# Kernel optimization log

Measured on AMD Instinct MI355X. Metric: run time of the kernel, lower is better.

## Reference

```python
import jax, jax.numpy as jnp
import numpy as np

NUM_HEADS = 4
NUM_GROUPS = 8
EPS = 1e-5


def setup_inputs() -> dict:
    key = jax.random.key(0)
    ks = jax.random.split(key, 7)
    c = 256
    return {
        "x": jax.random.normal(ks[0], (4, c, 64, 64), jnp.float32),
        "gn_w": jax.random.normal(ks[1], (c,), jnp.float32),
        "gn_b": jax.random.normal(ks[2], (c,), jnp.float32),
        "qkv_w": jax.random.normal(ks[3], (3 * c, c), jnp.float32) * (c ** -0.5),
        "qkv_b": jax.random.normal(ks[4], (3 * c,), jnp.float32) * 0.02,
        "proj_w": jax.random.normal(ks[5], (c, c), jnp.float32) * (c ** -0.5),
        "proj_b": jax.random.normal(ks[6], (c,), jnp.float32) * 0.02,
    }


def reference(x, gn_w, gn_b, qkv_w, qkv_b, proj_w, proj_b):
    b, c, h, w = x.shape
    n = h * w
    hd = c // NUM_HEADS

    # GroupNorm(8, c)
    xg = x.reshape(b, NUM_GROUPS, -1)
    mu = jnp.mean(xg, axis=-1, keepdims=True)
    var = jnp.var(xg, axis=-1, keepdims=True)
    xn = ((xg - mu) * jax.lax.rsqrt(var + EPS)).reshape(b, c, h, w)
    xn = xn * gn_w[:, None, None] + gn_b[:, None, None]

    # 1x1 conv == channel matmul
    qkv = jnp.einsum('oc,bchw->bohw', qkv_w, xn) + qkv_b[:, None, None]
    q, k, v = jnp.split(qkv, 3, axis=1)
    q = q.reshape(b, NUM_HEADS, hd, n)
    k = k.reshape(b, NUM_HEADS, hd, n)
    v = v.reshape(b, NUM_HEADS, hd, n)

    scale = hd ** (-0.5)
    attn = jax.nn.softmax(jnp.einsum('bhcn,bhcm->bhnm', q * scale, k), axis=-1)
    out = jnp.einsum('bhnm,bhcm->bhcn', attn, v).reshape(b, c, h, w)

    return x + jnp.einsum('oc,bchw->bohw', proj_w, out) + proj_b[:, None, None]
```

## Files before the change

kernel.cpp:

```cpp
#include <hip/hip_runtime.h>
#include <hip/hip_bf16.h>

typedef unsigned short u16;
typedef __attribute__((ext_vector_type(4))) float f32x4;
typedef __attribute__((ext_vector_type(16))) float f32x16;
typedef __attribute__((ext_vector_type(8))) __bf16 bf16x8;
typedef __attribute__((ext_vector_type(2))) unsigned u32x2;

#define DEVI static __device__ __forceinline__
#define MFMA32 __builtin_amdgcn_mfma_f32_32x32x16_bf16

#if defined(__has_builtin)
#if __has_builtin(__builtin_amdgcn_exp2f)
#define HAVE_EXP2 1
#endif
#endif

#ifdef HAVE_EXP2
#define EXPX(x) __builtin_amdgcn_exp2f(x)
#define QSCALE 0.18033688011112042f
#define THRX 11.5f
#else
#define EXPX(x) __expf(x)
#define QSCALE 0.125f
#define THRX 8.0f
#endif

DEVI u16 f2bf(float f) {
    union { float f; unsigned u; } v; v.f = f;
    unsigned r = v.u + 0x7fffu + ((v.u >> 16) & 1u);
    return (u16)(r >> 16);
}

DEVI unsigned cvtpk(float lo, float hi_) {
    unsigned r;
    asm("v_cvt_pk_bf16_f32 %0, %1, %2" : "=v"(r) : "v"(lo), "v"(hi_));
    return r;
}

DEVI void plswap(unsigned a, unsigned b, unsigned& o0, unsigned& o1) {
#if defined(__has_builtin) && __has_builtin(__builtin_amdgcn_permlane32_swap)
    u32x2 r = __builtin_amdgcn_permlane32_swap(a, b, false, false);
    o0 = r[0]; o1 = r[1];
#else
    unsigned xa = (unsigned)__shfl_xor((int)a, 32, 64);
    unsigned xb = (unsigned)__shfl_xor((int)b, 32, 64);
    bool hi = (threadIdx.x & 32) != 0;
    o0 = hi ? xb : a;
    o1 = hi ? b : xa;
#endif
}

DEVI void gld16(const u16* g, u16* l) {
    __builtin_amdgcn_global_load_lds(
        (const __attribute__((address_space(1))) unsigned int*)g,
        (__attribute__((address_space(3))) unsigned int*)l, 16, 0, 0);
}

__global__ void __launch_bounds__(256) gn_stats1_k(const float* __restrict__ x,
                                                   float* __restrict__ part) {
    int bid = blockIdx.x;
    int bg = bid >> 3, seg = bid & 7;
    const float4* p = reinterpret_cast<const float4*>(x + (size_t)bg * 131072 + seg * 16384);
    float s = 0.f, s2 = 0.f;
    for (int i = threadIdx.x; i < 4096; i += 256) {
        float4 v = p[i];
        s  += v.x + v.y + v.z + v.w;
        s2 += v.x * v.x + v.y * v.y + v.z * v.z + v.w * v.w;
    }
    for (int off = 32; off; off >>= 1) {
        s  += __shfl_down(s,  off, 64);
        s2 += __shfl_down(s2, off, 64);
    }
    __shared__ float sb[8];
    int w = threadIdx.x >> 6, l = threadIdx.x & 63;
    if (l == 0) { sb[w] = s; sb[4 + w] = s2; }
    __syncthreads();
    if (threadIdx.x == 0) {
        part[bid * 2]     = sb[0] + sb[1] + sb[2] + sb[3];
        part[bid * 2 + 1] = sb[4] + sb[5] + sb[6] + sb[7];
    }
}

__global__ void gn_stats2_k(const float* __restrict__ part, float* __restrict__ stats) {
    int t = threadIdx.x;
    if (t < 32) {
        float s = 0.f, s2 = 0.f;
#pragma unroll
        for (int i = 0; i < 8; i++) { s += part[(t * 8 + i) * 2]; s2 += part[(t * 8 + i) * 2 + 1]; }
        float mu  = s * (1.f / 131072.f);
        float var = s2 * (1.f / 131072.f) - mu * mu;
        stats[t * 2]     = mu;
        stats[t * 2 + 1] = rsqrtf(var + 1e-5f);
    }
}

__global__ void __launch_bounds__(256) convw_k(const float* __restrict__ qw,
                                               const float* __restrict__ pw,
                                               u16* __restrict__ wq,
                                               u16* __restrict__ wp) {
    int i = blockIdx.x * 256 + threadIdx.x;
    if (i < 196608) wq[i] = f2bf(qw[i]);
    if (i < 65536)  wp[i] = f2bf(pw[i]);
}

__global__ void __launch_bounds__(256) gnorm_t_k(const float* __restrict__ x,
                                                 const float* __restrict__ stats,
                                                 const float* __restrict__ gw,
                                                 const float* __restrict__ gb,
                                                 u16* __restrict__ xnT) {
    __shared__ float tile[32][33];
    int b = blockIdx.z, c0 = blockIdx.y * 32, n0 = blockIdx.x * 32;
    int tx = threadIdx.x, ty = threadIdx.y;
    const float* xb = x + ((size_t)b * 256 + c0) * 4096 + n0;
#pragma unroll
    for (int j = 0; j < 4; j++) {
        int r = ty + 8 * j;
        tile[r][tx] = xb[(size_t)r * 4096 + tx];
    }
    __syncthreads();
    int c = c0 + tx;
    int g = c >> 5;
    float mu = stats[(b * 8 + g) * 2], rs = stats[(b * 8 + g) * 2 + 1];
    float sc = rs * gw[c];
    float sh = gb[c] - mu * sc;
    u16* o = xnT + ((size_t)b * 4096 + n0) * 256 + c;
#pragma unroll
    for (int j = 0; j < 4; j++) {
        int r = ty + 8 * j;
        float v = tile[tx][r];
        o[(size_t)r * 256] = f2bf(v * sc + sh);
    }
}

__global__ void __launch_bounds__(256) qkv_gemm_k(const u16* __restrict__ wq,
                                                  const float* __restrict__ qkvb,
                                                  const u16* __restrict__ xnT,
                                                  u16* __restrict__ qT,
                                                  u16* __restrict__ kT,
                                                  u16* __restrict__ vv) {
    __shared__ __align__(16) u16 T[64 * 72];
    int b  = blockIdx.z;
    int w  = threadIdx.x >> 6, l = threadIdx.x & 63;
    int lr = l & 15, lg = l >> 4;
    int m0b = blockIdx.y * 64;
    int m0 = m0b + w * 16;
    int n0 = blockIdx.x * 64;
    f32x4 acc[4];
#pragma unroll
    for (int g = 0; g < 4; g++) acc[g] = (f32x4){0.f, 0.f, 0.f, 0.f};
    const u16* ap = wq + (size_t)(m0 + lr) * 256 + 8 * lg;
    const u16* bp = xnT + ((size_t)b * 4096 + n0 + lr) * 256 + 8 * lg;
#pragma unroll 2
    for (int k0 = 0; k0 < 256; k0 += 32) {
        bf16x8 a = *reinterpret_cast<const bf16x8*>(ap + k0);
#pragma unroll
        for (int g = 0; g < 4; g++) {
            bf16x8 bb = *reinterpret_cast<const bf16x8*>(bp + (size_t)g * 16 * 256 + k0);
            acc[g] = __builtin_amdgcn_mfma_f32_16x16x32_bf16(a, bb, acc[g], 0, 0, 0);
        }
    }
    int sec  = m0b >> 8;
    int hsec = (m0b >> 6) & 3;
    float qs = (sec == 0) ? QSCALE : 1.f;
#pragma unroll
    for (int g = 0; g < 4; g++) {
        ushort4 pk;
#pragma unroll
        for (int j = 0; j < 4; j++) {
            int o = m0 + lg * 4 + j;
            float v = (acc[g][j] + qkvb[o]) * qs;
            ((u16*)&pk)[j] = f2bf(v);
        }
        if (sec < 2) {
            *(ushort4*)&T[(g * 16 + lr) * 72 + w * 16 + lg * 4] = pk;
        } else {
#pragma unroll
            for (int j = 0; j < 4; j++)
                T[(w * 16 + lg * 4 + j) * 72 + g * 16 + lr] = ((u16*)&pk)[j];
        }
    }
    __syncthreads();
    int row = threadIdx.x >> 2;
    u16* dst;
    if (sec < 2) {
        u16* base = (sec == 0 ? qT : kT);
        dst = base + ((size_t)(b * 4 + hsec) * 4096 + n0 + row) * 64;
    } else {
        dst = vv + ((size_t)(b * 4 + hsec) * 64 + row) * 4096 + n0;
    }
#pragma unroll
    for (int p = 0; p < 2; p++) {
        int c = (threadIdx.x & 3) + 4 * p;
        *(ulonglong2*)(dst + c * 8) = *(const ulonglong2*)&T[row * 72 + c * 8];
    }
}

__global__ void __launch_bounds__(256) attn_k(const u16* __restrict__ qT,
                                              const u16* __restrict__ kT,
                                              const u16* __restrict__ vv,
                                              u16* __restrict__ oT) {
    __shared__ __align__(16) u16 kbuf[2][4096];
    __shared__ __align__(16) u16 vbuf[2][4096];
    const int bh = blockIdx.y, b = bh >> 2, h = bh & 3;
    const int tid = threadIdx.x, w = tid >> 6, l = tid & 63;
    const int q5 = l & 31, hi = l >> 5;
    const int n0w = blockIdx.x * 128 + w * 32;
    const u16* qp = qT + (size_t)bh * 262144;
    const u16* kp = kT + (size_t)bh * 262144;
    const u16* vp = vv + (size_t)bh * 262144;

    const u16* qrow = qp + (size_t)(n0w + q5) * 64 + 8 * hi;
    bf16x8 qf[4];
    qf[0] = *(const bf16x8*)(qrow);
    qf[1] = *(const bf16x8*)(qrow + 16);
    qf[2] = *(const bf16x8*)(qrow + 32);
    qf[3] = *(const bf16x8*)(qrow + 48);

    const int pr = l >> 3, pc = l & 7;
    const int gswz = ((pc ^ pr) << 3);
    const u16* kgl = kp + (size_t)(16 * w + pr) * 64 + gswz;
    const u16* vgl = vp + (size_t)(16 * w + pr) * 4096 + gswz;
    const int lbase = 1024 * w;
    const int ksw = q5 & 7;

    f32x16 o0, o1;
#pragma unroll
    for (int r = 0; r < 16; ++r) { o0[r] = 0.f; o1[r] = 0.f; }
    float mrun = -3.0e38f, lsum = 0.f;

#define STAGE(BUF, IT)                                                        \
    {                                                                         \
        const u16* kt_ = kgl + (size_t)(IT) * 4096;                           \
        const u16* vt_ = vgl + (size_t)(IT) * 64;                             \
        gld16(kt_,         &kbuf[BUF][lbase]);                                \
        gld16(kt_ + 512,   &kbuf[BUF][lbase + 512]);                          \
        gld16(vt_,         &vbuf[BUF][lbase]);                                \
        gld16(vt_ + 32768, &vbuf[BUF][lbase + 512]);                          \
    }

    STAGE(0, 0);
    __syncthreads();

    int cur = 0;
    for (int it = 0; it < 64; ++it) {
        if (it < 63) STAGE(cur ^ 1, it + 1);
        const u16* kb = &kbuf[cur][q5 * 64];
        const u16* vb = &vbuf[cur][q5 * 64];
        f32x16 s0, s1;
#pragma unroll
        for (int r = 0; r < 16; ++r) { s0[r] = 0.f; s1[r] = 0.f; }
        __builtin_amdgcn_s_setprio(1);
#pragma unroll
        for (int st = 0; st < 4; ++st) {
            int ch = ((hi + 2 * st) ^ ksw) << 3;
            s0 = MFMA32(*(const bf16x8*)(kb + ch),        qf[st], s0, 0, 0, 0);
            s1 = MFMA32(*(const bf16x8*)(kb + 2048 + ch), qf[st], s1, 0, 0, 0);
        }
        __builtin_amdgcn_s_setprio(0);
        float pm = s0[0];
#pragma unroll
        for (int r = 1; r < 16; ++r) pm = fmaxf(pm, s0[r]);
#pragma unroll
        for (int r = 0; r < 16; ++r) pm = fmaxf(pm, s1[r]);
        pm = fmaxf(pm, __shfl_xor(pm, 32, 64));
        if (!__all(pm - mrun <= THRX)) {
            float mnew = fmaxf(mrun, pm);
            float al = EXPX(mrun - mnew);
            mrun = mnew;
            lsum *= al;
#pragma unroll
            for (int r = 0; r < 16; ++r) {
                float ar = __shfl(al, (r & 3) + 8 * (r >> 2) + 4 * hi, 64);
                o0[r] *= ar; o1[r] *= ar;
            }
        }
        float rs = 0.f;
#pragma unroll
        for (int r = 0; r < 16; ++r) { s0[r] = EXPX(s0[r] - mrun); rs += s0[r]; }
#pragma unroll
        for (int r = 0; r < 16; ++r) { s1[r] = EXPX(s1[r] - mrun); rs += s1[r]; }
        rs += __shfl_xor(rs, 32, 64);
        lsum += rs;
        unsigned c0 = cvtpk(s0[0], s0[1]),   c1 = cvtpk(s0[2], s0[3]);
        unsigned c2 = cvtpk(s0[4], s0[5]),   c3 = cvtpk(s0[6], s0[7]);
        unsigned c4 = cvtpk(s0[8], s0[9]),   c5 = cvtpk(s0[10], s0[11]);
        unsigned c6 = cvtpk(s0[12], s0[13]), c7 = cvtpk(s0[14], s0[15]);
        unsigned d0 = cvtpk(s1[0], s1[1]),   d1 = cvtpk(s1[2], s1[3]);
        unsigned d2 = cvtpk(s1[4], s1[5]),   d3 = cvtpk(s1[6], s1[7]);
        unsigned d4 = cvtpk(s1[8], s1[9]),   d5 = cvtpk(s1[10], s1[11]);
        unsigned d6 = cvtpk(s1[12], s1[13]), d7 = cvtpk(s1[14], s1[15]);
        unsigned x0a, x0b, y0a, y0b, x1a, x1b, y1a, y1b;
        unsigned x2a, x2b, y2a, y2b, x3a, x3b, y3a, y3b;
        plswap(c0, c2, x0a, x0b); plswap(c1, c3, y0a, y0b);
        plswap(c4, c6, x1a, x1b); plswap(c5, c7, y1a, y1b);
        plswap(d0, d2, x2a, x2b); plswap(d1, d3, y2a, y2b);
        plswap(d4, d6, x3a, x3b); plswap(d5, d7, y3a, y3b);
        union { unsigned u[4]; bf16x8 v; } pa0, pa1, pa2, pa3;
        pa0.u[0] = x0a; pa0.u[1] = y0a; pa0.u[2] = x0b; pa0.u[3] = y0b;
        pa1.u[0] = x1a; pa1.u[1] = y1a; pa1.u[2] = x1b; pa1.u[3] = y1b;
        pa2.u[0] = x2a; pa2.u[1] = y2a; pa2.u[2] = x2b; pa2.u[3] = y2b;
        pa3.u[0] = x3a; pa3.u[1] = y3a; pa3.u[2] = x3b; pa3.u[3] = y3b;
        __builtin_amdgcn_s_setprio(1);
        {
            int ch0 = ((0 + hi) ^ ksw) << 3;
            int ch1 = ((2 + hi) ^ ksw) << 3;
            int ch2 = ((4 + hi) ^ ksw) << 3;
            int ch3 = ((6 + hi) ^ ksw) << 3;
            o0 = MFMA32(pa0.v, *(const bf16x8*)(vb + ch0),        o0, 0, 0, 0);
            o1 = MFMA32(pa0.v, *(const bf16x8*)(vb + 2048 + ch0), o1, 0, 0, 0);
            o0 = MFMA32(pa1.v, *(const bf16x8*)(vb + ch1),        o0, 0, 0, 0);
            o1 = MFMA32(pa1.v, *(const bf16x8*)(vb + 2048 + ch1), o1, 0, 0, 0);
            o0 = MFMA32(pa2.v, *(const bf16x8*)(vb + ch2),        o0, 0, 0, 0);
            o1 = MFMA32(pa2.v, *(const bf16x8*)(vb + 2048 + ch2), o1, 0, 0, 0);
            o0 = MFMA32(pa3.v, *(const bf16x8*)(vb + ch3),        o0, 0, 0, 0);
            o1 = MFMA32(pa3.v, *(const bf16x8*)(vb + 2048 + ch3), o1, 0, 0, 0);
        }
        __builtin_amdgcn_s_setprio(0);
        __syncthreads();
        cur ^= 1;
    }
#undef STAGE
    float linv = 1.f / lsum;
    u16* ob = oT + ((size_t)b * 4096 + n0w) * 256 + h * 64 + q5;
#pragma unroll
    for (int r = 0; r < 16; ++r) {
        int qo = (r & 3) + 8 * (r >> 2) + 4 * hi;
        float lr_ = __shfl(linv, qo, 64);
        ob[(size_t)qo * 256]      = f2bf(o0[r] * lr_);
        ob[(size_t)qo * 256 + 32] = f2bf(o1[r] * lr_);
    }
}

__global__ void __launch_bounds__(256) proj_gemm_k(const u16* __restrict__ wp,
                                                   const float* __restrict__ pb,
                                                   const u16* __restrict__ oT,
                                                   const float* __restrict__ x,
                                                   float* __restrict__ out) {
    int b  = blockIdx.z;
    int w  = threadIdx.x >> 6, l = threadIdx.x & 63;
    int lr = l & 15, lg = l >> 4;
    int m0 = blockIdx.y * 64 + w * 16;
    int n0 = blockIdx.x * 64;
    f32x4 acc[4];
#pragma unroll
    for (int g = 0; g < 4; g++) acc[g] = (f32x4){0.f, 0.f, 0.f, 0.f};
    const u16* ap = wp + (size_t)(m0 + lr) * 256 + 8 * lg;
    const u16* bp = oT + ((size_t)b * 4096 + n0 + lr) * 256 + 8 * lg;
#pragma unroll 2
    for (int k0 = 0; k0 < 256; k0 += 32) {
        bf16x8 a = *reinterpret_cast<const bf16x8*>(ap + k0);
#pragma unroll
        for (int g = 0; g < 4; g++) {
            bf16x8 bb = *reinterpret_cast<const bf16x8*>(bp + (size_t)g * 16 * 256 + k0);
            acc[g] = __builtin_amdgcn_mfma_f32_16x16x32_bf16(a, bb, acc[g], 0, 0, 0);
        }
    }
#pragma unroll
    for (int g = 0; g < 4; g++)
#pragma unroll
        for (int j = 0; j < 4; j++) {
            int o = m0 + lg * 4 + j;
            int n = n0 + g * 16 + lr;
            size_t idx = ((size_t)b * 256 + o) * 4096 + n;
            out[idx] = x[idx] + pb[o] + acc[g][j];
        }
}

extern "C" void kernel_launch(void* const* d_in, const int* in_sizes, int n_in,
                              void* d_out, int out_size, void* d_ws, size_t ws_size,
                              hipStream_t stream) {
    const float* x      = (const float*)d_in[0];
    const float* gn_w   = (const float*)d_in[1];
    const float* gn_b   = (const float*)d_in[2];
    const float* qkv_w  = (const float*)d_in[3];
    const float* qkv_b  = (const float*)d_in[4];
    const float* proj_w = (const float*)d_in[5];
    const float* proj_b = (const float*)d_in[6];
    float* out = (float*)d_out;

    char* ws = (char*)d_ws;
    float* stats = (float*)(ws + 0);
    u16* wq  = (u16*)(ws + 256);
    u16* wp  = (u16*)(ws + 393472);
    u16* xnT = (u16*)(ws + 524544);
    u16* qT  = (u16*)(ws + 8913152);
    u16* kT  = (u16*)(ws + 17301760);
    u16* vv  = (u16*)(ws + 25690368);
    u16* oT  = (u16*)(ws + 34078976);
    float* part = (float*)(ws + 42467584);

    gn_stats1_k<<<dim3(256), dim3(256), 0, stream>>>(x, part);
    gn_stats2_k<<<dim3(1), dim3(64), 0, stream>>>(part, stats);
    convw_k<<<dim3(768), dim3(256), 0, stream>>>(qkv_w, proj_w, wq, wp);
    gnorm_t_k<<<dim3(128, 8, 4), dim3(32, 8), 0, stream>>>(x, stats, gn_w, gn_b, xnT);
    qkv_gemm_k<<<dim3(64, 12, 4), dim3(256), 0, stream>>>(wq, qkv_b, xnT, qT, kT, vv);
    attn_k<<<dim3(32, 16), dim3(256), 0, stream>>>(qT, kT, vv, oT);
    proj_gemm_k<<<dim3(64, 4, 4), dim3(256), 0, stream>>>(wp, proj_b, oT, x, out);
}
```

Baseline: 267.9 us.

## Split attention over key halves and merge partial results in a combine kernel

Splits the KV sequence of the attention kernel into two halves processed by separate blocks, doubling the grid from 512 to 1024 blocks so the GPU has more work to fill its compute units. Each half writes unnormalized bf16 partial outputs plus per-row max and sum, and a new combine kernel rescales and merges them into the final output. It also adds an occupancy hint to launch bounds, starts the first QK MFMA from a zero accumulator, and uses tree reductions for the row max and sum. The cost is an extra kernel launch, extra memory traffic for the partials, and extra bf16 rounding of unnormalized partial results. pA aliases oT, and the combine kernel reads and writes oT in place.

```diff
diff --git a/kernel.cpp b/kernel.cpp
--- a/kernel.cpp
+++ b/kernel.cpp
@@ -30,6 +30,10 @@
     union { float f; unsigned u; } v; v.f = f;
     unsigned r = v.u + 0x7fffu + ((v.u >> 16) & 1u);
     return (u16)(r >> 16);
+}
+
+DEVI float bfu2f(unsigned lo16shifted) {
+    union { unsigned u; float f; } v; v.u = lo16shifted; return v.f;
 }
 
 DEVI unsigned cvtpk(float lo, float hi_) {
@@ -196,16 +200,20 @@
     }
 }
 
-__global__ void __launch_bounds__(256) attn_k(const u16* __restrict__ qT,
-                                              const u16* __restrict__ kT,
-                                              const u16* __restrict__ vv,
-                                              u16* __restrict__ oT) {
+__global__ void __launch_bounds__(256, 4) attn_k(const u16* __restrict__ qT,
+                                                 const u16* __restrict__ kT,
+                                                 const u16* __restrict__ vv,
+                                                 u16* __restrict__ pA,
+                                                 u16* __restrict__ pB,
+                                                 float2* __restrict__ pml) {
     __shared__ __align__(16) u16 kbuf[2][4096];
     __shared__ __align__(16) u16 vbuf[2][4096];
     const int bh = blockIdx.y, b = bh >> 2, h = bh & 3;
+    const int qb = blockIdx.x >> 1, khalf = blockIdx.x & 1;
     const int tid = threadIdx.x, w = tid >> 6, l = tid & 63;
     const int q5 = l & 31, hi = l >> 5;
-    const int n0w = blockIdx.x * 128 + w * 32;
+    const int n0w = qb * 128 + w * 32;
+    const int kbase = khalf * 2048;
     const u16* qp = qT + (size_t)bh * 262144;
     const u16* kp = kT + (size_t)bh * 262144;
     const u16* vp = vv + (size_t)bh * 262144;
@@ -219,14 +227,14 @@
 
     const int pr = l >> 3, pc = l & 7;
     const int gswz = ((pc ^ pr) << 3);
-    const u16* kgl = kp + (size_t)(16 * w + pr) * 64 + gswz;
-    const u16* vgl = vp + (size_t)(16 * w + pr) * 4096 + gswz;
+    const u16* kgl = kp + (size_t)(kbase + 16 * w + pr) * 64 + gswz;
+    const u16* vgl = vp + (size_t)(16 * w + pr) * 4096 + kbase + gswz;
     const int lbase = 1024 * w;
     const int ksw = q5 & 7;
 
-    f32x16 o0, o1;
-#pragma unroll
-    for (int r = 0; r < 16; ++r) { o0[r] = 0.f; o1[r] = 0.f; }
+    f32x16 o0, o1, zz;
+#pragma unroll
+    for (int r = 0; r < 16; ++r) { o0[r] = 0.f; o1[r] = 0.f; zz[r] = 0.f; }
     float mrun = -3.0e38f, lsum = 0.f;
 
 #define STAGE(BUF, IT)                                                        \
@@ -243,26 +251,32 @@
     __syncthreads();
 
     int cur = 0;
-    for (int it = 0; it < 64; ++it) {
-        if (it < 63) STAGE(cur ^ 1, it + 1);
+    for (int it = 0; it < 32; ++it) {
+        if (it < 31) STAGE(cur ^ 1, it + 1);
         const u16* kb = &kbuf[cur][q5 * 64];
         const u16* vb = &vbuf[cur][q5 * 64];
         f32x16 s0, s1;
-#pragma unroll
-        for (int r = 0; r < 16; ++r) { s0[r] = 0.f; s1[r] = 0.f; }
         __builtin_amdgcn_s_setprio(1);
-#pragma unroll
-        for (int st = 0; st < 4; ++st) {
+        {
+            int ch = ((hi) ^ ksw) << 3;
+            s0 = MFMA32(*(const bf16x8*)(kb + ch),        qf[0], zz, 0, 0, 0);
+            s1 = MFMA32(*(const bf16x8*)(kb + 2048 + ch), qf[0], zz, 0, 0, 0);
+        }
+#pragma unroll
+        for (int st = 1; st < 4; ++st) {
             int ch = ((hi + 2 * st) ^ ksw) << 3;
             s0 = MFMA32(*(const bf16x8*)(kb + ch),        qf[st], s0, 0, 0, 0);
             s1 = MFMA32(*(const bf16x8*)(kb + 2048 + ch), qf[st], s1, 0, 0, 0);
         }
         __builtin_amdgcn_s_setprio(0);
-        float pm = s0[0];
-#pragma unroll
-        for (int r = 1; r < 16; ++r) pm = fmaxf(pm, s0[r]);
-#pragma unroll
-        for (int r = 0; r < 16; ++r) pm = fmaxf(pm, s1[r]);
+        float t[16];
+#pragma unroll
+        for (int r = 0; r < 16; ++r) t[r] = fmaxf(s0[r], s1[r]);
+#pragma unroll
+        for (int k = 8; k; k >>= 1)
+#pragma unroll
+            for (int i = 0; i < 16 && i < k; ++i) t[i] = fmaxf(t[i], t[i + k]);
+        float pm = t[0];
         pm = fmaxf(pm, __shfl_xor(pm, 32, 64));
         if (!__all(pm - mrun <= THRX)) {
             float mnew = fmaxf(mrun, pm);
@@ -275,11 +289,18 @@
                 o0[r] *= ar; o1[r] *= ar;
             }
         }
-        float rs = 0.f;
-#pragma unroll
-        for (int r = 0; r < 16; ++r) { s0[r] = EXPX(s0[r] - mrun); rs += s0[r]; }
-#pragma unroll
-        for (int r = 0; r < 16; ++r) { s1[r] = EXPX(s1[r] - mrun); rs += s1[r]; }
+#pragma unroll
+        for (int r = 0; r < 16; ++r) s0[r] = EXPX(s0[r] - mrun);
+#pragma unroll
+        for (int r = 0; r < 16; ++r) s1[r] = EXPX(s1[r] - mrun);
+        float u[16];
+#pragma unroll
+        for (int r = 0; r < 16; ++r) u[r] = s0[r] + s1[r];
+#pragma unroll
+        for (int k = 8; k; k >>= 1)
+#pragma unroll
+            for (int i = 0; i < 16 && i < k; ++i) u[i] += u[i + k];
+        float rs = u[0];
         rs += __shfl_xor(rs, 32, 64);
         lsum += rs;
         unsigned c0 = cvtpk(s0[0], s0[1]),   c1 = cvtpk(s0[2], s0[3]);
@@ -321,15 +342,46 @@
         cur ^= 1;
     }
 #undef STAGE
-    float linv = 1.f / lsum;
-    u16* ob = oT + ((size_t)b * 4096 + n0w) * 256 + h * 64 + q5;
+    u16* ob = (khalf ? pB : pA) + ((size_t)b * 4096 + n0w) * 256 + h * 64 + q5;
 #pragma unroll
     for (int r = 0; r < 16; ++r) {
         int qo = (r & 3) + 8 * (r >> 2) + 4 * hi;
-        float lr_ = __shfl(linv, qo, 64);
-        ob[(size_t)qo * 256]      = f2bf(o0[r] * lr_);
-        ob[(size_t)qo * 256 + 32] = f2bf(o1[r] * lr_);
-    }
+        ob[(size_t)qo * 256]      = f2bf(o0[r]);
+        ob[(size_t)qo * 256 + 32] = f2bf(o1[r]);
+    }
+    if (hi == 0)
+        pml[((size_t)khalf * 16 + bh) * 4096 + n0w + q5] = make_float2(mrun, lsum);
+}
+
+__global__ void __launch_bounds__(256) combine_k(const u16* __restrict__ pA,
+                                                 const u16* __restrict__ pB,
+                                                 const float2* __restrict__ pml,
+                                                 u16* __restrict__ oT) {
+    int idx = blockIdx.x * 32 + (threadIdx.x >> 3);
+    int bh = idx >> 12, n = idx & 4095;
+    int d0 = (threadIdx.x & 7) * 8;
+    float2 mA = pml[(size_t)bh * 4096 + n];
+    float2 mB = pml[(size_t)(16 + bh) * 4096 + n];
+    float M = fmaxf(mA.x, mB.x);
+    float a0 = EXPX(mA.x - M), a1 = EXPX(mB.x - M);
+    float linv = 1.f / (mA.y * a0 + mB.y * a1);
+    a0 *= linv; a1 *= linv;
+    size_t off = (size_t)idx * 256 + ((bh & 3) * 64 - ((size_t)(bh & 3) << 18)) + d0;
+    {
+        int b = bh >> 2, h = bh & 3;
+        off = ((size_t)b * 4096 + n) * 256 + h * 64 + d0;
+    }
+    uint4 A = *(const uint4*)(pA + off);
+    uint4 B = *(const uint4*)(pB + off);
+    unsigned out[4];
+#pragma unroll
+    for (int j = 0; j < 4; ++j) {
+        unsigned ua = ((const unsigned*)&A)[j], ub = ((const unsigned*)&B)[j];
+        float lo = bfu2f(ua << 16) * a0 + bfu2f(ub << 16) * a1;
+        float hh = bfu2f(ua & 0xffff0000u) * a0 + bfu2f(ub & 0xffff0000u) * a1;
+        out[j] = cvtpk(lo, hh);
+    }
+    *(uint4*)(oT + off) = *(uint4*)out;
 }
 
 __global__ void __launch_bounds__(256) proj_gemm_k(const u16* __restrict__ wp,
@@ -389,12 +441,15 @@
     u16* vv  = (u16*)(ws + 25690368);
     u16* oT  = (u16*)(ws + 34078976);
     float* part = (float*)(ws + 42467584);
+    u16* pB  = (u16*)(ws + 42469632);
+    float2* pml = (float2*)(ws + 50858240);
 
     gn_stats1_k<<<dim3(256), dim3(256), 0, stream>>>(x, part);
     gn_stats2_k<<<dim3(1), dim3(64), 0, stream>>>(part, stats);
     convw_k<<<dim3(768), dim3(256), 0, stream>>>(qkv_w, proj_w, wq, wp);
     gnorm_t_k<<<dim3(128, 8, 4), dim3(32, 8), 0, stream>>>(x, stats, gn_w, gn_b, xnT);
     qkv_gemm_k<<<dim3(64, 12, 4), dim3(256), 0, stream>>>(wq, qkv_b, xnT, qT, kT, vv);
-    attn_k<<<dim3(32, 16), dim3(256), 0, stream>>>(qT, kT, vv, oT);
+    attn_k<<<dim3(64, 16), dim3(256), 0, stream>>>(qT, kT, vv, oT, pB, pml);
+    combine_k<<<dim3(2048), dim3(256), 0, stream>>>(oT, pB, pml, oT);
     proj_gemm_k<<<dim3(64, 4, 4), dim3(256), 0, stream>>>(wp, proj_b, oT, x, out);
 }
```

Measured after the change: 266.2 us. No clear change (-0.6%).
